# Performance work log

Measured on AMD Instinct MI355X. Metric: run time of the kernel, lower is better.

## Reference

```python
import jax, jax.numpy as jnp
import numpy as np

T = S = 1024
B = 8
HID = 1024
H = 16
D = HID // H          # head_size = 64
RELK = 16             # max relative position (clip window)
NEG = -1e9


def setup_inputs() -> dict:
    key = jax.random.key(0)
    ks = jax.random.split(key, 12)
    inv = 1.0 / np.sqrt(HID)
    inp = {
        'q': jax.random.normal(ks[0], (T, B, HID), jnp.float32),
        'k': jax.random.normal(ks[1], (S, B, HID), jnp.float32),
        'v': jax.random.normal(ks[2], (S, B, HID), jnp.float32),
        # additive float mask (B,T,S): causal, masked positions = -1e9
        'mask': jnp.broadcast_to(jnp.triu(jnp.full((T, S), NEG, jnp.float32), k=1), (B, T, S)),
        'Wq': jax.random.normal(ks[3], (HID, HID), jnp.float32) * inv,
        'bq': jnp.zeros((HID,), jnp.float32),
        'Wk': jax.random.normal(ks[4], (HID, HID), jnp.float32) * inv,
        'bk': jnp.zeros((HID,), jnp.float32),
        'Wv': jax.random.normal(ks[5], (HID, HID), jnp.float32) * inv,
        'bv': jnp.zeros((HID,), jnp.float32),
        'Wo': jax.random.normal(ks[6], (HID, HID), jnp.float32) * inv,
        'bo': jnp.zeros((HID,), jnp.float32),
        'rel_k_table': jax.random.normal(ks[7], (2 * RELK + 1, D), jnp.float32) * 0.02,
        'rel_v_table': jax.random.normal(ks[8], (2 * RELK + 1, D), jnp.float32) * 0.02,
    }
    return inp


def _rel_index(t, s):
    # clipped relative position index (t, s) -> [0, 2*RELK]
    return jnp.clip(jnp.arange(s)[None, :] - jnp.arange(t)[:, None], -RELK, RELK) + RELK


def reference(q, k, v, mask, Wq, bq, Wk, bk, Wv, bv, Wo, bo, rel_k_table, rel_v_table):
    t, b, _ = q.shape
    scaling = D ** -0.5
    # projections; torch Linear: x @ W^T + b, here weights stored (in,out)
    qh = ((q @ Wq + bq) * scaling).reshape(t, b * H, D).transpose(1, 0, 2)  # (BH,T,D)
    kh = (k @ Wk + bk).reshape(-1, b * H, D).transpose(1, 0, 2)            # (BH,S,D)
    vh = (v @ Wv + bv).reshape(-1, b * H, D).transpose(1, 0, 2)            # (BH,S,D)
    s = kh.shape[1]

    score = jnp.einsum('ntd,nsd->nts', qh, kh)                 # (BH,T,S)
    idx = _rel_index(t, s)
    rel_k = rel_k_table[idx]                                   # (T,S,D)
    score = score + jnp.einsum('ntd,tsd->nts', qh, rel_k)      # relative-pos bias on scores

    score = (score.reshape(b, H, t, s) + mask[:, None]).reshape(b * H, t, s)
    attn = jax.nn.softmax(score, axis=-1)                      # dropout=0 (eval)

    o = jnp.einsum('nts,nsd->ntd', attn, vh)                   # (BH,T,D)
    rel_v = rel_v_table[idx]                                   # (T,S,D)
    o = o + jnp.einsum('nts,tsd->ntd', attn, rel_v)            # relative-pos bias on values

    o = o.transpose(1, 0, 2).reshape(t, b, H * D)              # (T,B,hidden)
    return o @ Wo + bo
```

## Files before the change

### kernel.cpp

```cpp
#include <hip/hip_runtime.h>

typedef unsigned short u16;
typedef __bf16 bf16x8 __attribute__((ext_vector_type(8)));
typedef __bf16 bf16x4v __attribute__((ext_vector_type(4)));
typedef short s16x4 __attribute__((ext_vector_type(4)));
typedef unsigned short u16x8 __attribute__((ext_vector_type(8)));
typedef unsigned short u16x4 __attribute__((ext_vector_type(4)));
typedef float f32x4 __attribute__((ext_vector_type(4)));


__device__ __forceinline__ u16 f2bf(float f) {
  return __builtin_bit_cast(u16, (__bf16)f);
}
__device__ __forceinline__ u16x8 pack_trunc8(float4 a, float4 b) {
  u16x8 t;
  t[0] = (u16)(__float_as_uint(a.x) >> 16); t[1] = (u16)(__float_as_uint(a.y) >> 16);
  t[2] = (u16)(__float_as_uint(a.z) >> 16); t[3] = (u16)(__float_as_uint(a.w) >> 16);
  t[4] = (u16)(__float_as_uint(b.x) >> 16); t[5] = (u16)(__float_as_uint(b.y) >> 16);
  t[6] = (u16)(__float_as_uint(b.z) >> 16); t[7] = (u16)(__float_as_uint(b.w) >> 16);
  return t;
}
__device__ __forceinline__ void barrier_lgkm() {
  __asm__ volatile("s_waitcnt lgkmcnt(0)\ns_barrier" ::: "memory");
}
typedef const __attribute__((address_space(1))) void* gas_ptr;
typedef __attribute__((address_space(3))) void* las_ptr;
__device__ __forceinline__ void load_lds16(const void* g, void* l) {
  __builtin_amdgcn_global_load_lds((gas_ptr)g, (las_ptr)l, 16, 0, 0);
}
__device__ __forceinline__ f32x4 mfma16(u16x4 a, u16x4 b, f32x4 c) {
#if __has_builtin(__builtin_amdgcn_mfma_f32_16x16x16_bf16)
  return __builtin_amdgcn_mfma_f32_16x16x16_bf16(
      __builtin_bit_cast(bf16x4v, a), __builtin_bit_cast(bf16x4v, b), c, 0, 0, 0);
#elif __has_builtin(__builtin_amdgcn_mfma_f32_16x16x16bf16_1k)
  return __builtin_amdgcn_mfma_f32_16x16x16bf16_1k(
      __builtin_bit_cast(s16x4, a), __builtin_bit_cast(s16x4, b), c, 0, 0, 0);
#else
  f32x4 d;
  __asm__ volatile("v_mfma_f32_16x16x16_bf16 %0, %1, %2, %3"
                   : "=v"(d) : "v"(a), "v"(b), "v"(c));
  return d;
#endif
}

__device__ __forceinline__ void transpose_body(const float* in, u16* out) {
  __shared__ u16 tile[64][65];
  const int r0 = blockIdx.y * 64, c0 = blockIdx.x * 64;
  const int tid = threadIdx.x;
  const int tr = tid >> 4, tc4 = (tid & 15) * 4;
#pragma unroll
  for (int p = 0; p < 4; ++p) {
    int r = tr + p * 16;
    float4 vv = *(const float4*)&in[(size_t)(r0 + r) * 1024 + c0 + tc4];
    tile[r][tc4 + 0] = f2bf(vv.x); tile[r][tc4 + 1] = f2bf(vv.y);
    tile[r][tc4 + 2] = f2bf(vv.z); tile[r][tc4 + 3] = f2bf(vv.w);
  }
  __syncthreads();
#pragma unroll
  for (int p = 0; p < 4; ++p) {
    int rr = tr + p * 16;
    ushort4 ov;
    ov.x = tile[tc4 + 0][rr]; ov.y = tile[tc4 + 1][rr];
    ov.z = tile[tc4 + 2][rr]; ov.w = tile[tc4 + 3][rr];
    *(ushort4*)&out[(size_t)(c0 + rr) * 1024 + r0 + tc4] = ov;
  }
}
__global__ __launch_bounds__(256) void transpose_cvt3_kernel(
    const float* w0, const float* w1, const float* w2,
    u16* o0, u16* o1, u16* o2)
{
  const float* in = blockIdx.z == 0 ? w0 : (blockIdx.z == 1 ? w1 : w2);
  u16* out = blockIdx.z == 0 ? o0 : (blockIdx.z == 1 ? o1 : o2);
  transpose_body(in, out);
}
__global__ __launch_bounds__(256) void transpose_cvt_kernel(
    const float* in, u16* out) { transpose_body(in, out); }

__global__ __launch_bounds__(256) void cvt3_kernel(
    const float* __restrict__ a, const float* __restrict__ b,
    const float* __restrict__ c,
    u16* __restrict__ oa, u16* __restrict__ ob, u16* __restrict__ oc)
{
  const float* in = blockIdx.z == 0 ? a : (blockIdx.z == 1 ? b : c);
  u16* out = blockIdx.z == 0 ? oa : (blockIdx.z == 1 ? ob : oc);
  const int n8 = (8192 * 1024) / 8;
  for (int i = blockIdx.x * 256 + threadIdx.x; i < n8; i += gridDim.x * 256) {
    float4 x = ((const float4*)in)[i * 2];
    float4 y = ((const float4*)in)[i * 2 + 1];
    *(u16x8*)&out[(size_t)i * 8] = pack_trunc8(x, y);
  }
}

struct GemmArgs {
  const u16* A; const u16* BT; const float* bias; void* out;
  float scale; int mode;
};

__global__ __launch_bounds__(256) void gemm_lds_kernel(GemmArgs g0, GemmArgs g1)
{
  __shared__ __align__(16) u16 smem[128 * 136];
  const GemmArgs g = blockIdx.z ? g1 : g0;
  const u16* __restrict__ A = g.A;
  const u16* __restrict__ BT = g.BT;
  const int tid = threadIdx.x;
  const int wave = tid >> 6, lane = tid & 63;
  const int quad = lane >> 4, l16 = lane & 15;
  const int wave_m = wave >> 1, wave_n = wave & 1;
  const int m0 = blockIdx.x * 128, n0 = blockIdx.y * 128;

  const int crow = tid >> 2;
  const int cq = (((tid & 3) ^ ((tid >> 3) & 3))) * 8;
  const int qswr = (quad ^ ((l16 >> 1) & 3)) * 8;

  f32x4 acc[4][4] = {};

  auto STAGE = [&](int bo, int kb) {
    const size_t ka = (size_t)kb * 32 + cq;
    load_lds16(&A [(size_t)(m0 + crow)      * 1024 + ka], &smem[bo + tid * 8]);
    load_lds16(&A [(size_t)(m0 + 64 + crow) * 1024 + ka], &smem[bo + 2048 + tid * 8]);
    load_lds16(&BT[(size_t)(n0 + crow)      * 1024 + ka], &smem[bo + 4096 + tid * 8]);
    load_lds16(&BT[(size_t)(n0 + 64 + crow) * 1024 + ka], &smem[bo + 6144 + tid * 8]);
  };

  STAGE(0, 0);
  __syncthreads();
  int cur = 0;
  for (int kb = 0; kb < 32; ++kb) {
    if (kb + 1 < 32) STAGE(cur ^ 8192, kb + 1);
    const u16* As = &smem[cur];
    const u16* Bs = &smem[cur + 4096];
    bf16x8 af[4], bfr[4];
#pragma unroll
    for (int mt = 0; mt < 4; ++mt)
      af[mt] = *(const bf16x8*)&As[(wave_m * 64 + mt * 16 + l16) * 32 + qswr];
#pragma unroll
    for (int nt = 0; nt < 4; ++nt)
      bfr[nt] = *(const bf16x8*)&Bs[(wave_n * 64 + nt * 16 + l16) * 32 + qswr];
#pragma unroll
    for (int mt = 0; mt < 4; ++mt)
#pragma unroll
      for (int nt = 0; nt < 4; ++nt)
        acc[mt][nt] = __builtin_amdgcn_mfma_f32_16x16x32_bf16(af[mt], bfr[nt], acc[mt][nt], 0, 0, 0);
    __syncthreads();
    cur ^= 8192;
  }

  const float scale = g.scale;
  if (g.mode == 0) {
#pragma unroll
    for (int mt = 0; mt < 4; ++mt)
#pragma unroll
      for (int nt = 0; nt < 4; ++nt) {
        int nn = n0 + wave_n * 64 + nt * 16 + l16;
        float bval = g.bias[nn];
#pragma unroll
        for (int reg = 0; reg < 4; ++reg) {
          int mm = m0 + wave_m * 64 + mt * 16 + quad * 4 + reg;
          ((float*)g.out)[(size_t)mm * 1024 + nn] = (acc[mt][nt][reg] + bval) * scale;
        }
      }
  } else {
    __syncthreads();
    u16* Cs = smem;
#pragma unroll
    for (int mt = 0; mt < 4; ++mt)
#pragma unroll
      for (int nt = 0; nt < 4; ++nt) {
        int nnl = wave_n * 64 + nt * 16 + l16;
        float bval = g.bias[n0 + nnl];
#pragma unroll
        for (int reg = 0; reg < 4; ++reg) {
          int mml = wave_m * 64 + mt * 16 + quad * 4 + reg;
          Cs[mml * 136 + nnl] = f2bf((acc[mt][nt][reg] + bval) * scale);
        }
      }
    __syncthreads();
    u16* out = (u16*)g.out;
    if (g.mode == 1) {
      int row = tid >> 1, half = tid & 1;
      int mm = m0 + row;
      int tt = mm >> 3, bbv = mm & 7;
      int hh = (n0 >> 6) + half;
      u16* dst = &out[(((size_t)(bbv * 16 + hh)) * 1024 + tt) * 64];
#pragma unroll
      for (int i = 0; i < 8; ++i)
        *(u16x8*)&dst[i * 8] = *(const u16x8*)&Cs[row * 136 + half * 64 + i * 8];
    } else {
      int t0 = m0 >> 3;
#pragma unroll
      for (int rr = 0; rr < 4; ++rr) {
        int rid = tid * 4 + rr;
        int nnv = rid >> 3, bbv = rid & 7;
        int hh = (n0 + nnv) >> 6, dd = (n0 + nnv) & 63;
        u16* dst = &out[(((size_t)(bbv * 16 + hh)) * 64 + dd) * 1024 + t0];
        u16x8 w0, w1;
#pragma unroll
        for (int t = 0; t < 8; ++t) w0[t] = Cs[(t * 8 + bbv) * 136 + nnv];
#pragma unroll
        for (int t = 0; t < 8; ++t) w1[t] = Cs[((t + 8) * 8 + bbv) * 136 + nnv];
        *(u16x8*)&dst[0] = w0;
        *(u16x8*)&dst[8] = w1;
      }
    }
  }
}

__global__ __launch_bounds__(256, 4) void attn_kernel(
    const u16* __restrict__ qh, const u16* __restrict__ kh,
    const u16* __restrict__ vt, const float* __restrict__ relk,
    const float* __restrict__ relv, u16* __restrict__ octx)
{
  const int n = blockIdx.x;
  const int q0 = (15 - blockIdx.y) * 64;
  const int tid = threadIdx.x;
  const int wave = tid >> 6, lane = tid & 63;
  const int quad = lane >> 4, l16 = lane & 15;
  const int rowi = wave * 16 + l16;
  const int trow = q0 + rowi;
  const float LOG2E = 1.442695040888963f;

  __shared__ __align__(16) u16 Ks[64 * 72];
  __shared__ __align__(16) u16 Vs[64 * 72];
  __shared__ float qrelS[64 * 17];
  __shared__ float wvS[17 * 64];
  __shared__ float relvS[17 * 64];

  const int diag = q0 >> 6;
  const int ntiles = diag + 1;

  bf16x8 qf[2];
#pragma unroll
  for (int kc = 0; kc < 2; ++kc)
    qf[kc] = *(const bf16x8*)&qh[((size_t)n * 1024 + trow) * 64 + kc * 32 + quad * 8];

  const u16* __restrict__ khn = kh + (size_t)n * 1024 * 64;
  const u16* __restrict__ vtn = vt + (size_t)n * 64 * 1024;

  u16x8 kA[2], vA[2], kB[2], vB[2];
  auto LOADT = [&](int s0, u16x8 (&kr)[2], u16x8 (&vr)[2]) {
#pragma unroll
    for (int j = 0; j < 2; ++j) {
      int c = j * 256 + tid;
      kr[j] = *(const u16x8*)&khn[(size_t)(s0 + (c >> 3)) * 64 + (c & 7) * 8];
      vr[j] = *(const u16x8*)&vtn[(size_t)(c >> 3) * 1024 + s0 + (c & 7) * 8];
    }
  };
  LOADT(0, kA, vA);
  if (1 < ntiles) LOADT(64, kB, vB);

  for (int i = tid; i < 17 * 64; i += 256) { wvS[i] = relk[i]; relvS[i] = relv[i]; }
  __syncthreads();

  float qreg[16];
#pragma unroll
  for (int kc = 0; kc < 2; ++kc)
#pragma unroll
    for (int jj = 0; jj < 8; ++jj)
      qreg[kc * 8 + jj] = (float)qf[kc][jj];
  float qrel0 = 0.f;
  for (int r = 0; r <= 16; ++r) {
    float s = 0.f;
#pragma unroll
    for (int kc = 0; kc < 2; ++kc)
#pragma unroll
      for (int jj = 0; jj < 8; ++jj)
        s += qreg[kc * 8 + jj] * wvS[r * 64 + kc * 32 + quad * 8 + jj];
    s += __shfl_xor(s, 16);
    s += __shfl_xor(s, 32);
    float sv = (s - 8.f) * LOG2E;
    if (r == 0) qrel0 = sv;
    if (quad == 0) qrelS[rowi * 17 + r] = sv;
  }
  __syncthreads();
  for (int i = tid; i < 17 * 64; i += 256) wvS[i] = 0.f;
  __syncthreads();

  f32x4 oacc[4] = {};
  float lrow = 0.f;

  auto WRITET = [&](u16x8 (&kr)[2], u16x8 (&vr)[2]) {
#pragma unroll
    for (int j = 0; j < 2; ++j) {
      int c = j * 256 + tid;
      *(u16x8*)&Ks[(c >> 3) * 72 + (c & 7) * 8] = kr[j];
      *(u16x8*)&Vs[(c >> 3) * 72 + (c & 7) * 8] = vr[j];
    }
  };

  auto COMPUTE = [&](int st) {
    const int s0 = st * 64;
    f32x4 sc[4];
#pragma unroll
    for (int j = 0; j < 4; ++j) {
      f32x4 c4 = {};
#pragma unroll
      for (int kc = 0; kc < 2; ++kc) {
        bf16x8 kf = *(const bf16x8*)&Ks[(j * 16 + l16) * 72 + kc * 32 + quad * 8];
        c4 = __builtin_amdgcn_mfma_f32_16x16x32_bf16(kf, qf[kc], c4, 0, 0, 0);
      }
      sc[j] = c4;
    }

    u16x4 pfrag[4];
    if (st < diag - 1) {
#pragma unroll
      for (int j = 0; j < 4; ++j) {
        u16x4 pk;
#pragma unroll
        for (int reg = 0; reg < 4; ++reg) {
          float pv = exp2f(fmaf(sc[j][reg], LOG2E, qrel0));
          lrow += pv;
          pk[reg] = f2bf(pv);
        }
        pfrag[j] = pk;
      }
    } else {
#pragma unroll
      for (int j = 0; j < 4; ++j) {
        u16x4 pk;
#pragma unroll
        for (int reg = 0; reg < 4; ++reg) {
          int sel = s0 + j * 16 + quad * 4 + reg;
          int dt = trow - sel;
          float pv = 0.f;
          if (dt >= 0) {
            int r = (dt < 16) ? (16 - dt) : 0;
            pv = exp2f(fmaf(sc[j][reg], LOG2E, qrelS[rowi * 17 + r]));
            if (dt < 16) wvS[rowi * 17 + (16 - dt)] = pv;
          }
          lrow += pv;
          pk[reg] = f2bf(pv);
        }
        pfrag[j] = pk;
      }
    }

#pragma unroll
    for (int nt = 0; nt < 4; ++nt)
#pragma unroll
      for (int j = 0; j < 4; ++j) {
        u16x4 vfrag = *(const u16x4*)&Vs[(nt * 16 + l16) * 72 + j * 16 + quad * 4];
        oacc[nt] = mfma16(vfrag, pfrag[j], oacc[nt]);
      }
  };

  for (int st = 0; st < ntiles; st += 2) {
    if (st) barrier_lgkm();
    WRITET(kA, vA);
    barrier_lgkm();
    if (st + 2 < ntiles) LOADT((st + 2) * 64, kA, vA);
    COMPUTE(st);
    if (st + 1 >= ntiles) break;
    barrier_lgkm();
    WRITET(kB, vB);
    barrier_lgkm();
    if (st + 3 < ntiles) LOADT((st + 3) * 64, kB, vB);
    COMPUTE(st + 1);
  }

  lrow += __shfl_xor(lrow, 16);
  lrow += __shfl_xor(lrow, 32);

  float wvr[17];
  float bsum = 0.f;
#pragma unroll
  for (int r = 1; r <= 16; ++r) { wvr[r] = wvS[rowi * 17 + r]; bsum += wvr[r]; }
  wvr[0] = lrow - bsum;
  float linv = 1.f / lrow;

  const int hh = n & 15, bb = n >> 4;
  size_t base = ((size_t)trow * 8 + bb) * 1024 + hh * 64;
#pragma unroll
  for (int nt = 0; nt < 4; ++nt) {
    u16x4 ov;
#pragma unroll
    for (int reg = 0; reg < 4; ++reg) {
      int d = nt * 16 + quad * 4 + reg;
      float rv = 0.f;
#pragma unroll
      for (int r = 0; r <= 16; ++r) rv += wvr[r] * relvS[r * 64 + d];
      ov[reg] = f2bf((oacc[nt][reg] + rv) * linv);
    }
    *(u16x4*)&octx[base + nt * 16 + quad * 4] = ov;
  }
}

extern "C" void kernel_launch(void* const* d_in, const int* in_sizes, int n_in,
                              void* d_out, int out_size, void* d_ws, size_t ws_size,
                              hipStream_t stream) {
  (void)in_sizes; (void)n_in; (void)out_size; (void)ws_size;
  const float* q    = (const float*)d_in[0];
  const float* k    = (const float*)d_in[1];
  const float* v    = (const float*)d_in[2];
  const float* Wq   = (const float*)d_in[4];
  const float* bq   = (const float*)d_in[5];
  const float* Wk   = (const float*)d_in[6];
  const float* bk   = (const float*)d_in[7];
  const float* Wv   = (const float*)d_in[8];
  const float* bv   = (const float*)d_in[9];
  const float* Wo   = (const float*)d_in[10];
  const float* bo   = (const float*)d_in[11];
  const float* relk = (const float*)d_in[12];
  const float* relv = (const float*)d_in[13];
  float* out = (float*)d_out;

  char* ws = (char*)d_ws;
  u16* vt   = (u16*)(ws);
  u16* qh   = (u16*)(ws + ((size_t)16 << 20));
  u16* kh   = (u16*)(ws + ((size_t)32 << 20));
  u16* vbf  = kh;
  u16* octx = (u16*)(ws + ((size_t)48 << 20));
  u16* wqt  = (u16*)(ws + ((size_t)48 << 20));
  u16* wkt  = (u16*)(ws + ((size_t)50 << 20));
  u16* wvt  = (u16*)(ws + ((size_t)52 << 20));
  u16* wot  = kh;
  u16* qbf  = (u16*)d_out;
  u16* kbf  = (u16*)d_out + ((size_t)8 << 20);

  dim3 blk(256);
  transpose_cvt3_kernel<<<dim3(16, 16, 3), blk, 0, stream>>>(Wq, Wk, Wv, wqt, wkt, wvt);

  cvt3_kernel<<<dim3(2048, 1, 3), blk, 0, stream>>>(q, k, v, qbf, kbf, vbf);

  GemmArgs gv{vbf, wvt, bv, vt, 1.0f, 2};
  gemm_lds_kernel<<<dim3(64, 8, 1), blk, 0, stream>>>(gv, gv);

  GemmArgs gq{qbf, wqt, bq, qh, 0.125f, 1};
  GemmArgs gk{kbf, wkt, bk, kh, 1.0f,   1};
  gemm_lds_kernel<<<dim3(64, 8, 2), blk, 0, stream>>>(gq, gk);

  attn_kernel<<<dim3(128, 16), blk, 0, stream>>>(qh, kh, vt, relk, relv, octx);

  transpose_cvt_kernel<<<dim3(16, 16), blk, 0, stream>>>(Wo, wot);

  GemmArgs go{octx, wot, bo, out, 1.0f, 0};
  gemm_lds_kernel<<<dim3(64, 8, 1), blk, 0, stream>>>(go, go);
}
```

Baseline: 360.5 us.

## Shrink GEMM M-tile to 64 and issue prefetch after fragment loads; vectorize V reads

```diff
diff --git a/kernel.cpp b/kernel.cpp
--- a/kernel.cpp
+++ b/kernel.cpp
@@ -22,6 +22,10 @@
 }
 __device__ __forceinline__ void barrier_lgkm() {
   __asm__ volatile("s_waitcnt lgkmcnt(0)\ns_barrier" ::: "memory");
+}
+__device__ __forceinline__ void barrier_vm() {
+  __asm__ volatile("s_waitcnt vmcnt(0)" ::: "memory");
+  __builtin_amdgcn_s_barrier();
 }
 typedef const __attribute__((address_space(1))) void* gas_ptr;
 typedef __attribute__((address_space(3))) void* las_ptr;
@@ -96,9 +100,9 @@
   float scale; int mode;
 };
 
-__global__ __launch_bounds__(256) void gemm_lds_kernel(GemmArgs g0, GemmArgs g1)
+__global__ __launch_bounds__(256, 4) void gemm_lds_kernel(GemmArgs g0, GemmArgs g1)
 {
-  __shared__ __align__(16) u16 smem[128 * 136];
+  __shared__ __align__(16) u16 smem[12288];
   const GemmArgs g = blockIdx.z ? g1 : g0;
   const u16* __restrict__ A = g.A;
   const u16* __restrict__ BT = g.BT;
@@ -106,85 +110,84 @@
   const int wave = tid >> 6, lane = tid & 63;
   const int quad = lane >> 4, l16 = lane & 15;
   const int wave_m = wave >> 1, wave_n = wave & 1;
-  const int m0 = blockIdx.x * 128, n0 = blockIdx.y * 128;
+  const int m0 = blockIdx.x * 64, n0 = blockIdx.y * 128;
 
   const int crow = tid >> 2;
   const int cq = (((tid & 3) ^ ((tid >> 3) & 3))) * 8;
   const int qswr = (quad ^ ((l16 >> 1) & 3)) * 8;
 
-  f32x4 acc[4][4] = {};
+  f32x4 acc[2][4] = {};
 
   auto STAGE = [&](int bo, int kb) {
     const size_t ka = (size_t)kb * 32 + cq;
     load_lds16(&A [(size_t)(m0 + crow)      * 1024 + ka], &smem[bo + tid * 8]);
-    load_lds16(&A [(size_t)(m0 + 64 + crow) * 1024 + ka], &smem[bo + 2048 + tid * 8]);
-    load_lds16(&BT[(size_t)(n0 + crow)      * 1024 + ka], &smem[bo + 4096 + tid * 8]);
-    load_lds16(&BT[(size_t)(n0 + 64 + crow) * 1024 + ka], &smem[bo + 6144 + tid * 8]);
+    load_lds16(&BT[(size_t)(n0 + crow)      * 1024 + ka], &smem[bo + 2048 + tid * 8]);
+    load_lds16(&BT[(size_t)(n0 + 64 + crow) * 1024 + ka], &smem[bo + 4096 + tid * 8]);
   };
 
   STAGE(0, 0);
-  __syncthreads();
+  barrier_vm();
   int cur = 0;
   for (int kb = 0; kb < 32; ++kb) {
-    if (kb + 1 < 32) STAGE(cur ^ 8192, kb + 1);
     const u16* As = &smem[cur];
-    const u16* Bs = &smem[cur + 4096];
-    bf16x8 af[4], bfr[4];
-#pragma unroll
-    for (int mt = 0; mt < 4; ++mt)
-      af[mt] = *(const bf16x8*)&As[(wave_m * 64 + mt * 16 + l16) * 32 + qswr];
+    const u16* Bs = &smem[cur + 2048];
+    bf16x8 af[2], bfr[4];
+#pragma unroll
+    for (int mt = 0; mt < 2; ++mt)
+      af[mt] = *(const bf16x8*)&As[(wave_m * 32 + mt * 16 + l16) * 32 + qswr];
 #pragma unroll
     for (int nt = 0; nt < 4; ++nt)
       bfr[nt] = *(const bf16x8*)&Bs[(wave_n * 64 + nt * 16 + l16) * 32 + qswr];
-#pragma unroll
-    for (int mt = 0; mt < 4; ++mt)
+    if (kb + 1 < 32) STAGE(cur ^ 6144, kb + 1);
+#pragma unroll
+    for (int mt = 0; mt < 2; ++mt)
 #pragma unroll
       for (int nt = 0; nt < 4; ++nt)
         acc[mt][nt] = __builtin_amdgcn_mfma_f32_16x16x32_bf16(af[mt], bfr[nt], acc[mt][nt], 0, 0, 0);
-    __syncthreads();
-    cur ^= 8192;
+    barrier_vm();
+    cur ^= 6144;
   }
 
   const float scale = g.scale;
   if (g.mode == 0) {
 #pragma unroll
-    for (int mt = 0; mt < 4; ++mt)
+    for (int mt = 0; mt < 2; ++mt)
 #pragma unroll
       for (int nt = 0; nt < 4; ++nt) {
         int nn = n0 + wave_n * 64 + nt * 16 + l16;
         float bval = g.bias[nn];
 #pragma unroll
         for (int reg = 0; reg < 4; ++reg) {
-          int mm = m0 + wave_m * 64 + mt * 16 + quad * 4 + reg;
+          int mm = m0 + wave_m * 32 + mt * 16 + quad * 4 + reg;
           ((float*)g.out)[(size_t)mm * 1024 + nn] = (acc[mt][nt][reg] + bval) * scale;
         }
       }
   } else {
-    __syncthreads();
     u16* Cs = smem;
 #pragma unroll
-    for (int mt = 0; mt < 4; ++mt)
+    for (int mt = 0; mt < 2; ++mt)
 #pragma unroll
       for (int nt = 0; nt < 4; ++nt) {
         int nnl = wave_n * 64 + nt * 16 + l16;
         float bval = g.bias[n0 + nnl];
 #pragma unroll
         for (int reg = 0; reg < 4; ++reg) {
-          int mml = wave_m * 64 + mt * 16 + quad * 4 + reg;
+          int mml = wave_m * 32 + mt * 16 + quad * 4 + reg;
           Cs[mml * 136 + nnl] = f2bf((acc[mt][nt][reg] + bval) * scale);
         }
       }
     __syncthreads();
     u16* out = (u16*)g.out;
     if (g.mode == 1) {
-      int row = tid >> 1, half = tid & 1;
+      int run = tid >> 1, sub = tid & 1;
+      int row = run >> 1, half = run & 1;
       int mm = m0 + row;
       int tt = mm >> 3, bbv = mm & 7;
       int hh = (n0 >> 6) + half;
-      u16* dst = &out[(((size_t)(bbv * 16 + hh)) * 1024 + tt) * 64];
-#pragma unroll
-      for (int i = 0; i < 8; ++i)
-        *(u16x8*)&dst[i * 8] = *(const u16x8*)&Cs[row * 136 + half * 64 + i * 8];
+      u16* dst = &out[(((size_t)(bbv * 16 + hh)) * 1024 + tt) * 64 + sub * 32];
+#pragma unroll
+      for (int i = 0; i < 4; ++i)
+        *(u16x8*)&dst[i * 8] = *(const u16x8*)&Cs[row * 136 + half * 64 + sub * 32 + i * 8];
     } else {
       int t0 = m0 >> 3;
 #pragma unroll
@@ -193,13 +196,10 @@
         int nnv = rid >> 3, bbv = rid & 7;
         int hh = (n0 + nnv) >> 6, dd = (n0 + nnv) & 63;
         u16* dst = &out[(((size_t)(bbv * 16 + hh)) * 64 + dd) * 1024 + t0];
-        u16x8 w0, w1;
+        u16x8 w0;
 #pragma unroll
         for (int t = 0; t < 8; ++t) w0[t] = Cs[(t * 8 + bbv) * 136 + nnv];
-#pragma unroll
-        for (int t = 0; t < 8; ++t) w1[t] = Cs[((t + 8) * 8 + bbv) * 136 + nnv];
         *(u16x8*)&dst[0] = w0;
-        *(u16x8*)&dst[8] = w1;
       }
     }
   }
@@ -283,7 +283,13 @@
     for (int j = 0; j < 2; ++j) {
       int c = j * 256 + tid;
       *(u16x8*)&Ks[(c >> 3) * 72 + (c & 7) * 8] = kr[j];
-      *(u16x8*)&Vs[(c >> 3) * 72 + (c & 7) * 8] = vr[j];
+      int d = c >> 3, c7 = c & 7;
+      int vbase = d * 72 + (c7 & 1) * 32 + (c7 >> 1) * 4;
+      u16x8 vv = vr[j];
+      u16x4 vlo = {vv[0], vv[1], vv[2], vv[3]};
+      u16x4 vhi = {vv[4], vv[5], vv[6], vv[7]};
+      *(u16x4*)&Vs[vbase]      = vlo;
+      *(u16x4*)&Vs[vbase + 16] = vhi;
     }
   };
 
@@ -336,12 +342,16 @@
     }
 
 #pragma unroll
-    for (int nt = 0; nt < 4; ++nt)
-#pragma unroll
-      for (int j = 0; j < 4; ++j) {
-        u16x4 vfrag = *(const u16x4*)&Vs[(nt * 16 + l16) * 72 + j * 16 + quad * 4];
-        oacc[nt] = mfma16(vfrag, pfrag[j], oacc[nt]);
-      }
+    for (int nt = 0; nt < 4; ++nt) {
+#pragma unroll
+      for (int jp = 0; jp < 2; ++jp) {
+        u16x8 vv = *(const u16x8*)&Vs[(nt * 16 + l16) * 72 + quad * 16 + jp * 8];
+        u16x4 vlo = {vv[0], vv[1], vv[2], vv[3]};
+        u16x4 vhi = {vv[4], vv[5], vv[6], vv[7]};
+        oacc[nt] = mfma16(vlo, pfrag[jp * 2],     oacc[nt]);
+        oacc[nt] = mfma16(vhi, pfrag[jp * 2 + 1], oacc[nt]);
+      }
+    }
   };
 
   for (int st = 0; st < ntiles; st += 2) {
@@ -423,16 +433,16 @@
   cvt3_kernel<<<dim3(2048, 1, 3), blk, 0, stream>>>(q, k, v, qbf, kbf, vbf);
 
   GemmArgs gv{vbf, wvt, bv, vt, 1.0f, 2};
-  gemm_lds_kernel<<<dim3(64, 8, 1), blk, 0, stream>>>(gv, gv);
+  gemm_lds_kernel<<<dim3(128, 8, 1), blk, 0, stream>>>(gv, gv);
 
   GemmArgs gq{qbf, wqt, bq, qh, 0.125f, 1};
   GemmArgs gk{kbf, wkt, bk, kh, 1.0f,   1};
-  gemm_lds_kernel<<<dim3(64, 8, 2), blk, 0, stream>>>(gq, gk);
+  gemm_lds_kernel<<<dim3(128, 8, 2), blk, 0, stream>>>(gq, gk);
 
   attn_kernel<<<dim3(128, 16), blk, 0, stream>>>(qh, kh, vt, relk, relv, octx);
 
   transpose_cvt_kernel<<<dim3(16, 16), blk, 0, stream>>>(Wo, wot);
 
   GemmArgs go{octx, wot, bo, out, 1.0f, 0};
-  gemm_lds_kernel<<<dim3(64, 8, 1), blk, 0, stream>>>(go, go);
-}
+  gemm_lds_kernel<<<dim3(128, 8, 1), blk, 0, stream>>>(go, go);
+}
```

Result: slower. 368.2 us (+2.1%).

## Triple-buffer GEMM LDS staging and permute V layout for wide fragment reads

Applied to the files above, without the earlier changes.

```diff
diff --git a/kernel.cpp b/kernel.cpp
--- a/kernel.cpp
+++ b/kernel.cpp
@@ -96,9 +96,9 @@
   float scale; int mode;
 };
 
-__global__ __launch_bounds__(256) void gemm_lds_kernel(GemmArgs g0, GemmArgs g1)
+__global__ __launch_bounds__(256, 3) void gemm_lds_kernel(GemmArgs g0, GemmArgs g1)
 {
-  __shared__ __align__(16) u16 smem[128 * 136];
+  __shared__ __align__(16) u16 smem[24576];
   const GemmArgs g = blockIdx.z ? g1 : g0;
   const u16* __restrict__ A = g.A;
   const u16* __restrict__ BT = g.BT;
@@ -122,13 +122,17 @@
     load_lds16(&BT[(size_t)(n0 + 64 + crow) * 1024 + ka], &smem[bo + 6144 + tid * 8]);
   };
 
-  STAGE(0, 0);
-  __syncthreads();
-  int cur = 0;
+  int b0 = 0, b1 = 8192, b2 = 16384;
+  STAGE(b0, 0);
+  STAGE(b1, 1);
   for (int kb = 0; kb < 32; ++kb) {
-    if (kb + 1 < 32) STAGE(cur ^ 8192, kb + 1);
-    const u16* As = &smem[cur];
-    const u16* Bs = &smem[cur + 4096];
+    if (kb < 31)
+      __asm__ volatile("s_waitcnt vmcnt(4) lgkmcnt(0)\ns_barrier" ::: "memory");
+    else
+      __asm__ volatile("s_waitcnt vmcnt(0) lgkmcnt(0)\ns_barrier" ::: "memory");
+    if (kb + 2 < 32) STAGE(b2, kb + 2);
+    const u16* As = &smem[b0];
+    const u16* Bs = &smem[b0 + 4096];
     bf16x8 af[4], bfr[4];
 #pragma unroll
     for (int mt = 0; mt < 4; ++mt)
@@ -141,8 +145,7 @@
 #pragma unroll
       for (int nt = 0; nt < 4; ++nt)
         acc[mt][nt] = __builtin_amdgcn_mfma_f32_16x16x32_bf16(af[mt], bfr[nt], acc[mt][nt], 0, 0, 0);
-    __syncthreads();
-    cur ^= 8192;
+    int t = b0; b0 = b1; b1 = b2; b2 = t;
   }
 
   const float scale = g.scale;
@@ -283,7 +286,13 @@
     for (int j = 0; j < 2; ++j) {
       int c = j * 256 + tid;
       *(u16x8*)&Ks[(c >> 3) * 72 + (c & 7) * 8] = kr[j];
-      *(u16x8*)&Vs[(c >> 3) * 72 + (c & 7) * 8] = vr[j];
+      int d = c >> 3, c7 = c & 7;
+      int vbase = d * 72 + (c7 & 1) * 32 + (c7 >> 1) * 4;
+      u16x8 vv = vr[j];
+      u16x4 vlo = {vv[0], vv[1], vv[2], vv[3]};
+      u16x4 vhi = {vv[4], vv[5], vv[6], vv[7]};
+      *(u16x4*)&Vs[vbase]      = vlo;
+      *(u16x4*)&Vs[vbase + 16] = vhi;
     }
   };
 
@@ -336,12 +345,16 @@
     }
 
 #pragma unroll
-    for (int nt = 0; nt < 4; ++nt)
-#pragma unroll
-      for (int j = 0; j < 4; ++j) {
-        u16x4 vfrag = *(const u16x4*)&Vs[(nt * 16 + l16) * 72 + j * 16 + quad * 4];
-        oacc[nt] = mfma16(vfrag, pfrag[j], oacc[nt]);
-      }
+    for (int nt = 0; nt < 4; ++nt) {
+#pragma unroll
+      for (int jp = 0; jp < 2; ++jp) {
+        u16x8 vv = *(const u16x8*)&Vs[(nt * 16 + l16) * 72 + quad * 16 + jp * 8];
+        u16x4 vlo = {vv[0], vv[1], vv[2], vv[3]};
+        u16x4 vhi = {vv[4], vv[5], vv[6], vv[7]};
+        oacc[nt] = mfma16(vlo, pfrag[jp * 2],     oacc[nt]);
+        oacc[nt] = mfma16(vhi, pfrag[jp * 2 + 1], oacc[nt]);
+      }
+    }
   };
 
   for (int st = 0; st < ntiles; st += 2) {
```

After: 339.3 us. 5.9% less time.
